# Kernel optimization log

Measured on AMD Instinct MI355X. Metric: run time of the kernel, lower is better.

## Reference

```python
import jax, jax.numpy as jnp
import numpy as np

B, C, H, W = 32, 256, 32, 32   # batch, channels (inplanes==planes), spatial
E = 8                          # num_experts
EPS = 1e-5                     # BatchNorm eps


def setup_inputs() -> dict:
    key = jax.random.key(0)
    ks = jax.random.split(key, 6)
    s = 0.05
    return {
        "x": jax.random.normal(ks[0], (B, C, H, W), dtype=jnp.float32),
        # router: GAP -> Linear(C, E) -> sigmoid
        "router_w": jax.random.normal(ks[1], (E, C), dtype=jnp.float32) * s,
        "router_b": jnp.zeros((E,), dtype=jnp.float32),
        # expert kernel banks for the two CondConv2d layers (OIHW per expert)
        "w1": jax.random.normal(ks[2], (E, C, C, 3, 3), dtype=jnp.float32) * s,
        "w2": jax.random.normal(ks[3], (E, C, C, 3, 3), dtype=jnp.float32) * s,
        # BatchNorm (eval mode: running stats) params for bn1/bn2
        "g1": jnp.ones((C,), jnp.float32), "b1": jnp.zeros((C,), jnp.float32),
        "m1": jnp.zeros((C,), jnp.float32), "v1": jnp.ones((C,), jnp.float32),
        "g2": jnp.ones((C,), jnp.float32), "b2": jnp.zeros((C,), jnp.float32),
        "m2": jnp.zeros((C,), jnp.float32), "v2": jnp.ones((C,), jnp.float32),
    }


def _bn(x, g, b, m, v):
    # eval-mode BatchNorm over channel dim 1
    scale = (g * jax.lax.rsqrt(v + EPS))[None, :, None, None]
    shift = (b - m * g * jax.lax.rsqrt(v + EPS))[None, :, None, None]
    return x * scale + shift


def _cond_conv(x, w_bank, r):
    # x: [B,C,H,W]; w_bank: [E,O,I,3,3]; r: [B,E]
    # combine expert kernels per sample, then per-sample 3x3 conv (pad=1, stride=1)
    k = jnp.einsum('be,eoihw->boihw', r, w_bank)  # [B,O,I,3,3]

    def one(xb, kb):
        return jax.lax.conv_general_dilated(
            xb[None], kb, window_strides=(1, 1), padding=[(1, 1), (1, 1)],
            dimension_numbers=('NCHW', 'OIHW', 'NCHW'))[0]

    return jax.vmap(one)(x, k)  # [B,O,H,W]


def reference(x, router_w, router_b, w1, w2, g1, b1, m1, v1, g2, b2, m2, v2):
    # BasicRouter: global average pool -> linear -> sigmoid
    r = jax.nn.sigmoid(jnp.mean(x, axis=(2, 3)) @ router_w.T + router_b)  # [B,E]
    # drop_expert is identity in eval mode (training=False)
    out = jax.nn.relu(_bn(_cond_conv(x, w1, r), g1, b1, m1, v1))
    out = _bn(_cond_conv(out, w2, r), g2, b2, m2, v2)
    return jax.nn.relu(out + x)  # identity residual (stride=1, inplanes==planes)
```

## Files before the change

kernel.cpp:

```cpp
#include <hip/hip_runtime.h>

typedef unsigned short ushort_t;
typedef __attribute__((ext_vector_type(8))) __bf16 bf16x8;
typedef __attribute__((ext_vector_type(4))) float f32x4;
typedef __attribute__((ext_vector_type(4))) int i32x4;
typedef __attribute__((ext_vector_type(4))) unsigned short u16x4;

#define BN_EPS 1e-5f
#define EPAD 136

#define BAR()    __builtin_amdgcn_s_barrier()
#define VMCNT4() asm volatile("s_waitcnt vmcnt(4)" ::: "memory")
#define VMCNT0() asm volatile("s_waitcnt vmcnt(0)" ::: "memory")
#define LGKM0()  asm volatile("s_waitcnt lgkmcnt(0)" ::: "memory")

__device__ __forceinline__ ushort_t f2bf(float f) {
    union { float f; unsigned u; } v; v.f = f;
    unsigned r = v.u + 0x7FFFu + ((v.u >> 16) & 1u);
    return (ushort_t)(r >> 16);
}
__device__ __forceinline__ float bf2f(ushort_t h) {
    union { unsigned u; float f; } v; v.u = ((unsigned)h) << 16; return v.f;
}

__device__ __forceinline__ void async_cp16(const ushort_t* g, ushort_t* l) {
    __builtin_amdgcn_global_load_lds(
        (const __attribute__((address_space(1))) unsigned int*)g,
        (__attribute__((address_space(3))) unsigned int*)l, 16, 0, 0);
}

__global__ void transpose_gap_kernel(const float* __restrict__ x, ushort_t* __restrict__ xt,
                                     float* __restrict__ gpart) {
    __shared__ float tile[32][33];
    int b = blockIdx.z, c0 = blockIdx.y * 32, p0 = blockIdx.x * 32;
    int t = threadIdx.x;
    int c = t >> 3, q = t & 7;
    f32x4 v = *(const f32x4*)(x + ((long)b * 256 + c0 + c) * 1024 + p0 + q * 4);
    tile[c][q * 4 + 0] = v[0];
    tile[c][q * 4 + 1] = v[1];
    tile[c][q * 4 + 2] = v[2];
    tile[c][q * 4 + 3] = v[3];
    float ps = v[0] + v[1] + v[2] + v[3];
    ps += __shfl_down(ps, 4, 8);
    ps += __shfl_down(ps, 2, 8);
    ps += __shfl_down(ps, 1, 8);
    if (q == 0) gpart[((long)b * 256 + c0 + c) * 32 + blockIdx.x] = ps;
    __syncthreads();
    int p = t >> 3, coff = (t & 7) * 4;
    u16x4 pk;
    #pragma unroll
    for (int i = 0; i < 4; ++i) pk[i] = f2bf(tile[coff + i][p]);
    *(u16x4*)(xt + ((long)b * 1024 + p0 + p) * 256 + c0 + coff) = pk;
}

__global__ void router_linear_kernel(const float* __restrict__ gpart, const float* __restrict__ rw,
                                     const float* __restrict__ rb, float* __restrict__ r) {
    int be = blockIdx.x;
    int b = be >> 3, e = be & 7;
    int lane = threadIdx.x;
    float s = 0.f;
    #pragma unroll
    for (int i = 0; i < 4; ++i) {
        int c = lane + i * 64;
        const f32x4* gp = (const f32x4*)(gpart + ((long)b * 256 + c) * 32);
        float g = 0.f;
        #pragma unroll
        for (int j = 0; j < 8; ++j) { f32x4 v = gp[j]; g += (v[0] + v[1]) + (v[2] + v[3]); }
        s += g * rw[e * 256 + c];
    }
    #pragma unroll
    for (int off = 32; off; off >>= 1) s += __shfl_down(s, off, 64);
    if (lane == 0) r[be] = 1.f / (1.f + expf(-(s * (1.f / 1024.f) + rb[e])));
}

__global__ __launch_bounds__(256, 2) void combine_kernel(const float* __restrict__ w,
                                                         const float* __restrict__ r,
                                                         ushort_t* __restrict__ ko) {
    __shared__ float wl[9216];
    ushort_t* outb = (ushort_t*)wl;
    const int t = threadIdx.x;
    const int g0 = blockIdx.x * 128;

    #pragma unroll
    for (int it = 0; it < 9; ++it) {
        int lin = it * 256 + t;
        int e = lin / 288, rem = lin - e * 288;
        f32x4 v = *(const f32x4*)(w + (long)e * 589824 + (long)g0 * 9 + rem * 4);
        *(f32x4*)(&wl[lin * 4]) = v;
    }
    __syncthreads();

    const int g = t & 127;
    const int half = t >> 7;
    float wv[8][9];
    #pragma unroll
    for (int e = 0; e < 8; ++e)
        #pragma unroll
        for (int p = 0; p < 9; ++p)
            wv[e][p] = wl[e * 1152 + g * 9 + p];
    __syncthreads();

    #pragma unroll
    for (int hb = 0; hb < 2; ++hb) {
        #pragma unroll
        for (int j = 0; j < 8; ++j) {
            int b16 = half * 8 + j;
            int b = hb * 16 + b16;
            float rv[8];
            #pragma unroll
            for (int e = 0; e < 8; ++e) rv[e] = r[b * 8 + e];
            #pragma unroll
            for (int p = 0; p < 9; ++p) {
                float s = 0.f;
                #pragma unroll
                for (int e = 0; e < 8; ++e) s += rv[e] * wv[e][p];
                outb[(b16 * 9 + p) * 128 + g] = f2bf(s);
            }
        }
        __syncthreads();
        #pragma unroll
        for (int it = 0; it < 9; ++it) {
            int idx = it * 256 + t;
            int row = idx >> 4, off = idx & 15;
            int b16 = row / 9, p = row - b16 * 9;
            i32x4 v = *(i32x4*)(&outb[row * 128 + off * 8]);
            *(i32x4*)(ko + ((long)((hb * 16 + b16) * 9 + p)) * 65536 + g0 + off * 8) = v;
        }
        __syncthreads();
    }
}

template <int MODE>
__global__ __launch_bounds__(256, 2) void gemm_conv(
    const ushort_t* __restrict__ xin,
    const ushort_t* __restrict__ kbank,
    void* __restrict__ outp,
    const float* __restrict__ gam, const float* __restrict__ bet,
    const float* __restrict__ mu, const float* __restrict__ var,
    const ushort_t* __restrict__ residt) {
    __shared__ ushort_t smem[37632];
    ushort_t* ldsB = smem;
    ushort_t* ldsA = smem + 13056;

    const int t = threadIdx.x;
    const int lane = t & 63;
    const int lane15 = lane & 15;
    const int quad = lane >> 4;
    const int wv = t >> 6;
    const int id = blockIdx.x;
    const int q  = id >> 3;
    const int mt = q & 1;
    const int nt = (q >> 1) & 7;
    const int b  = (id & 7) + ((q >> 4) << 3);
    const int h0 = nt * 4;
    const int p0 = nt * 128;
    const int mw0 = (wv >> 1) * 64;
    const int nw0 = (wv & 1) * 64;
    const int wbase = t & ~63;

    f32x4 acc[4][4];
    #pragma unroll
    for (int i = 0; i < 4; ++i)
        #pragma unroll
        for (int j = 0; j < 4; ++j) acc[i][j] = 0.f;

    if (t < 96) {
        int rix = t >> 3, j = t & 7;
        int pi = (rix >> 1) * 34 + (rix & 1) * 33;
        i32x4 z = 0;
        *(i32x4*)(&ldsB[(pi * 8 + j) * 8]) = z;
    }
    if (nt == 0) { i32x4 z = 0; *(i32x4*)(&ldsB[(8 + t) * 8]) = z; }
    if (nt == 7) { i32x4 z = 0; *(i32x4*)(&ldsB[((5 * 34 + 1) * 8 + t) * 8]) = z; }

    const long xbase = (long)b * 1024 * 256;
    const long kbase = (long)b * 9 * 65536;

    auto stageB = [&](int kc) {
        #pragma unroll
        for (int hh = 0; hh < 6; ++hh) {
            int hg = h0 + hh - 1;
            if (hg < 0 || hg >= 32) continue;
            int ww = t >> 3;
            int pi = hh * 34 + 1 + ww;
            int jd = (t & 7) ^ (pi & 7);
            async_cp16(xin + xbase + (long)(hg * 32 + ww) * 256 + kc * 64 + jd * 8,
                       ldsB + ((hh * 34 + 1) * 8 + wbase) * 8);
        }
    };
    auto stageA = [&](int kc, int pos, int buf) {
        const ushort_t* srcA = kbank + kbase + (long)pos * 65536 + (long)mt * 32768 + kc * 64;
        ushort_t* base = ldsA + buf * 8192;
        #pragma unroll
        for (int it = 0; it < 4; ++it) {
            int s = it * 256 + t;
            int row = s >> 3;
            int k8 = (s & 7) ^ (row & 7);
            async_cp16(srcA + (long)row * 256 + k8 * 8, base + (it * 256 + wbase) * 8);
        }
    };

    stageB(0);
    stageA(0, 0, 0);
    __syncthreads();

    int cur = 0;
    for (int kc = 0; kc < 4; ++kc) {
        for (int pos = 0; pos < 9; ++pos) {
            const bool last = (kc == 3 && pos == 8);
            const int nxt = (cur == 2) ? 0 : cur + 1;
            if (!last) {
                int nk = kc, np = pos + 1;
                if (np == 9) { np = 0; ++nk; }
                stageA(nk, np, nxt);
                VMCNT4();
            } else {
                VMCNT0();
            }
            BAR();

            const int dh = pos / 3 - 1, dw = pos % 3 - 1;
            const ushort_t* ab = ldsA + cur * 8192;
            bf16x8 af[2][4], bfr[2][4];
            #pragma unroll
            for (int kb = 0; kb < 2; ++kb) {
                int jk = kb * 4 + quad;
                #pragma unroll
                for (int mf = 0; mf < 4; ++mf) {
                    int row = mw0 + mf * 16 + lane15;
                    af[kb][mf] = *(const bf16x8*)(ab + (row * 8 + (jk ^ (row & 7))) * 8);
                }
                #pragma unroll
                for (int nf = 0; nf < 4; ++nf) {
                    int n = nw0 + nf * 16 + lane15;
                    int pi = ((n >> 5) + 1 + dh) * 34 + (n & 31) + 1 + dw;
                    bfr[kb][nf] = *(const bf16x8*)(&ldsB[(pi * 8 + (jk ^ (pi & 7))) * 8]);
                }
            }
            if (pos == 8 && kc < 3) {
                LGKM0();
                BAR();
                stageB(kc + 1);
            }

            __builtin_amdgcn_s_setprio(1);
            #pragma unroll
            for (int kb = 0; kb < 2; ++kb)
                #pragma unroll
                for (int mf = 0; mf < 4; ++mf)
                    #pragma unroll
                    for (int nf = 0; nf < 4; ++nf)
                        acc[mf][nf] = __builtin_amdgcn_mfma_f32_16x16x32_bf16(af[kb][mf], bfr[kb][nf], acc[mf][nf], 0, 0, 0);
            __builtin_amdgcn_s_setprio(0);
            LGKM0();
            cur = nxt;
        }
    }

    u16x4 rres[4][4];
    if (MODE == 1) {
        #pragma unroll
        for (int mf = 0; mf < 4; ++mf)
            #pragma unroll
            for (int nf = 0; nf < 4; ++nf) {
                int p = p0 + nw0 + nf * 16 + lane15;
                int cb = mt * 128 + mw0 + mf * 16 + quad * 4;
                rres[mf][nf] = *(const u16x4*)(residt + ((long)b * 1024 + p) * 256 + cb);
            }
    }

    float sc[4][4], sh[4][4];
    #pragma unroll
    for (int mf = 0; mf < 4; ++mf)
        #pragma unroll
        for (int i = 0; i < 4; ++i) {
            int c = mt * 128 + mw0 + mf * 16 + quad * 4 + i;
            float s = gam[c] * rsqrtf(var[c] + BN_EPS);
            sc[mf][i] = s;
            sh[mf][i] = bet[c] - mu[c] * s;
        }

    if (MODE == 0) {
        __syncthreads();
        ushort_t* ldsE = smem;
        #pragma unroll
        for (int mf = 0; mf < 4; ++mf)
            #pragma unroll
            for (int nf = 0; nf < 4; ++nf) {
                int pl = nw0 + nf * 16 + lane15;
                int cb = mw0 + mf * 16 + quad * 4;
                u16x4 pk;
                #pragma unroll
                for (int i = 0; i < 4; ++i) {
                    float v = acc[mf][nf][i] * sc[mf][i] + sh[mf][i];
                    pk[i] = f2bf(fmaxf(v, 0.f));
                }
                *(u16x4*)(&ldsE[pl * EPAD + cb]) = pk;
            }
        __syncthreads();
        ushort_t* op = (ushort_t*)outp;
        #pragma unroll
        for (int it = 0; it < 8; ++it) {
            int s = t + it * 256;
            int row = s >> 4, l16 = s & 15;
            i32x4 v = *(i32x4*)(&ldsE[row * EPAD + l16 * 8]);
            *(i32x4*)(op + ((long)b * 1024 + p0 + row) * 256 + mt * 128 + l16 * 8) = v;
        }
    } else {
        float* op = (float*)outp;
        #pragma unroll
        for (int mf = 0; mf < 4; ++mf)
            #pragma unroll
            for (int nf = 0; nf < 4; ++nf) {
                int p = p0 + nw0 + nf * 16 + lane15;
                #pragma unroll
                for (int i = 0; i < 4; ++i) {
                    int c = mt * 128 + mw0 + mf * 16 + quad * 4 + i;
                    float v = acc[mf][nf][i] * sc[mf][i] + sh[mf][i] + bf2f(rres[mf][nf][i]);
                    op[((long)b * 256 + c) * 1024 + p] = fmaxf(v, 0.f);
                }
            }
    }
}

extern "C" void kernel_launch(void* const* d_in, const int* in_sizes, int n_in,
                              void* d_out, int out_size, void* d_ws, size_t ws_size,
                              hipStream_t stream) {
    const float* x  = (const float*)d_in[0];
    const float* rw = (const float*)d_in[1];
    const float* rb = (const float*)d_in[2];
    const float* w1 = (const float*)d_in[3];
    const float* w2 = (const float*)d_in[4];
    const float* g1 = (const float*)d_in[5];
    const float* b1 = (const float*)d_in[6];
    const float* m1 = (const float*)d_in[7];
    const float* v1 = (const float*)d_in[8];
    const float* g2 = (const float*)d_in[9];
    const float* b2 = (const float*)d_in[10];
    const float* m2 = (const float*)d_in[11];
    const float* v2 = (const float*)d_in[12];

    const size_t GP_OFF  = 4096;
    const size_t XT_OFF  = GP_OFF + (size_t)1048576;
    const size_t O1_OFF  = XT_OFF + (size_t)16777216;
    const size_t KB_OFF  = O1_OFF + (size_t)16777216;
    const size_t NEED    = KB_OFF + (size_t)32 * 9 * 65536 * 2;
    if (ws_size < NEED) return;

    char* ws = (char*)d_ws;
    float* r       = (float*)ws;
    float* gpart   = (float*)(ws + GP_OFF);
    ushort_t* xt   = (ushort_t*)(ws + XT_OFF);
    ushort_t* o1   = (ushort_t*)(ws + O1_OFF);
    ushort_t* kbuf = (ushort_t*)(ws + KB_OFF);

    transpose_gap_kernel<<<dim3(32, 8, 32), 256, 0, stream>>>(x, xt, gpart);
    router_linear_kernel<<<256, 64, 0, stream>>>(gpart, rw, rb, r);
    combine_kernel<<<dim3(512), 256, 0, stream>>>(w1, r, kbuf);
    gemm_conv<0><<<512, 256, 0, stream>>>(xt, kbuf, (void*)o1, g1, b1, m1, v1, nullptr);
    combine_kernel<<<dim3(512), 256, 0, stream>>>(w2, r, kbuf);
    gemm_conv<1><<<512, 256, 0, stream>>>(o1, kbuf, d_out, g2, b2, m2, v2, xt);
}
```

Baseline: 227.4 us.

## Use two-wave blocks with 128x64 warp tiles and double-buffered weight staging

Shrinks the conv GEMM block from four waves to two, so each wave computes a 128x64 tile (8x4 MFMA fragments) instead of 64x64, and each A fragment is reused across more B columns. The weight pipeline goes from a triple buffer to a double buffer to cut LDS use, with an extra barrier every step to guard buffer reuse. This aims to raise MFMA work per LDS read, but doubles accumulator registers per thread and halves the waves per block. That can reduce latency hiding and may cause spills under the new launch bounds.

```diff
diff --git a/kernel.cpp b/kernel.cpp
--- a/kernel.cpp
+++ b/kernel.cpp
@@ -10,7 +10,7 @@
 #define EPAD 136
 
 #define BAR()    __builtin_amdgcn_s_barrier()
-#define VMCNT4() asm volatile("s_waitcnt vmcnt(4)" ::: "memory")
+#define VMCNT8() asm volatile("s_waitcnt vmcnt(8)" ::: "memory")
 #define VMCNT0() asm volatile("s_waitcnt vmcnt(0)" ::: "memory")
 #define LGKM0()  asm volatile("s_waitcnt lgkmcnt(0)" ::: "memory")
 
@@ -131,14 +131,14 @@
 }
 
 template <int MODE>
-__global__ __launch_bounds__(256, 2) void gemm_conv(
+__global__ __launch_bounds__(128, 1) void gemm_conv(
     const ushort_t* __restrict__ xin,
     const ushort_t* __restrict__ kbank,
     void* __restrict__ outp,
     const float* __restrict__ gam, const float* __restrict__ bet,
     const float* __restrict__ mu, const float* __restrict__ var,
     const ushort_t* __restrict__ residt) {
-    __shared__ ushort_t smem[37632];
+    __shared__ ushort_t smem[29440];
     ushort_t* ldsB = smem;
     ushort_t* ldsA = smem + 13056;
 
@@ -146,7 +146,7 @@
     const int lane = t & 63;
     const int lane15 = lane & 15;
     const int quad = lane >> 4;
-    const int wv = t >> 6;
+    const int wvi = t >> 6;
     const int id = blockIdx.x;
     const int q  = id >> 3;
     const int mt = q & 1;
@@ -154,13 +154,12 @@
     const int b  = (id & 7) + ((q >> 4) << 3);
     const int h0 = nt * 4;
     const int p0 = nt * 128;
-    const int mw0 = (wv >> 1) * 64;
-    const int nw0 = (wv & 1) * 64;
+    const int nw0 = wvi * 64;
     const int wbase = t & ~63;
 
-    f32x4 acc[4][4];
-    #pragma unroll
-    for (int i = 0; i < 4; ++i)
+    f32x4 acc[8][4];
+    #pragma unroll
+    for (int i = 0; i < 8; ++i)
         #pragma unroll
         for (int j = 0; j < 4; ++j) acc[i][j] = 0.f;
 
@@ -170,8 +169,16 @@
         i32x4 z = 0;
         *(i32x4*)(&ldsB[(pi * 8 + j) * 8]) = z;
     }
-    if (nt == 0) { i32x4 z = 0; *(i32x4*)(&ldsB[(8 + t) * 8]) = z; }
-    if (nt == 7) { i32x4 z = 0; *(i32x4*)(&ldsB[((5 * 34 + 1) * 8 + t) * 8]) = z; }
+    if (nt == 0) {
+        i32x4 z = 0;
+        *(i32x4*)(&ldsB[(8 + t) * 8]) = z;
+        *(i32x4*)(&ldsB[(8 + 128 + t) * 8]) = z;
+    }
+    if (nt == 7) {
+        i32x4 z = 0;
+        *(i32x4*)(&ldsB[((5 * 34 + 1) * 8 + t) * 8]) = z;
+        *(i32x4*)(&ldsB[((5 * 34 + 1) * 8 + 128 + t) * 8]) = z;
+    }
 
     const long xbase = (long)b * 1024 * 256;
     const long kbase = (long)b * 9 * 65536;
@@ -181,22 +188,26 @@
         for (int hh = 0; hh < 6; ++hh) {
             int hg = h0 + hh - 1;
             if (hg < 0 || hg >= 32) continue;
-            int ww = t >> 3;
-            int pi = hh * 34 + 1 + ww;
-            int jd = (t & 7) ^ (pi & 7);
-            async_cp16(xin + xbase + (long)(hg * 32 + ww) * 256 + kc * 64 + jd * 8,
-                       ldsB + ((hh * 34 + 1) * 8 + wbase) * 8);
+            #pragma unroll
+            for (int rr = 0; rr < 2; ++rr) {
+                int s = rr * 128 + t;
+                int ww = s >> 3;
+                int pi = hh * 34 + 1 + ww;
+                int jd = (s & 7) ^ (pi & 7);
+                async_cp16(xin + xbase + (long)(hg * 32 + ww) * 256 + kc * 64 + jd * 8,
+                           ldsB + ((hh * 34 + 1) * 8 + rr * 128 + wbase) * 8);
+            }
         }
     };
     auto stageA = [&](int kc, int pos, int buf) {
         const ushort_t* srcA = kbank + kbase + (long)pos * 65536 + (long)mt * 32768 + kc * 64;
         ushort_t* base = ldsA + buf * 8192;
         #pragma unroll
-        for (int it = 0; it < 4; ++it) {
-            int s = it * 256 + t;
+        for (int it = 0; it < 8; ++it) {
+            int s = it * 128 + t;
             int row = s >> 3;
             int k8 = (s & 7) ^ (row & 7);
-            async_cp16(srcA + (long)row * 256 + k8 * 8, base + (it * 256 + wbase) * 8);
+            async_cp16(srcA + (long)row * 256 + k8 * 8, base + (it * 128 + wbase) * 8);
         }
     };
 
@@ -204,30 +215,31 @@
     stageA(0, 0, 0);
     __syncthreads();
 
-    int cur = 0;
+    int par = 0;
+    #pragma unroll 1
     for (int kc = 0; kc < 4; ++kc) {
+        #pragma unroll 1
         for (int pos = 0; pos < 9; ++pos) {
             const bool last = (kc == 3 && pos == 8);
-            const int nxt = (cur == 2) ? 0 : cur + 1;
             if (!last) {
                 int nk = kc, np = pos + 1;
                 if (np == 9) { np = 0; ++nk; }
-                stageA(nk, np, nxt);
-                VMCNT4();
+                stageA(nk, np, par ^ 1);
+                VMCNT8();
             } else {
                 VMCNT0();
             }
             BAR();
 
             const int dh = pos / 3 - 1, dw = pos % 3 - 1;
-            const ushort_t* ab = ldsA + cur * 8192;
-            bf16x8 af[2][4], bfr[2][4];
+            const ushort_t* ab = ldsA + par * 8192;
+            bf16x8 af[2][8], bfr[2][4];
             #pragma unroll
             for (int kb = 0; kb < 2; ++kb) {
                 int jk = kb * 4 + quad;
                 #pragma unroll
-                for (int mf = 0; mf < 4; ++mf) {
-                    int row = mw0 + mf * 16 + lane15;
+                for (int mf = 0; mf < 8; ++mf) {
+                    int row = mf * 16 + lane15;
                     af[kb][mf] = *(const bf16x8*)(ab + (row * 8 + (jk ^ (row & 7))) * 8);
                 }
                 #pragma unroll
@@ -237,44 +249,42 @@
                     bfr[kb][nf] = *(const bf16x8*)(&ldsB[(pi * 8 + (jk ^ (pi & 7))) * 8]);
                 }
             }
-            if (pos == 8 && kc < 3) {
-                LGKM0();
-                BAR();
-                stageB(kc + 1);
-            }
+            LGKM0();
+            BAR();
+
+            if (pos == 8 && kc < 3) stageB(kc + 1);
 
             __builtin_amdgcn_s_setprio(1);
             #pragma unroll
             for (int kb = 0; kb < 2; ++kb)
                 #pragma unroll
-                for (int mf = 0; mf < 4; ++mf)
+                for (int mf = 0; mf < 8; ++mf)
                     #pragma unroll
                     for (int nf = 0; nf < 4; ++nf)
                         acc[mf][nf] = __builtin_amdgcn_mfma_f32_16x16x32_bf16(af[kb][mf], bfr[kb][nf], acc[mf][nf], 0, 0, 0);
             __builtin_amdgcn_s_setprio(0);
-            LGKM0();
-            cur = nxt;
-        }
-    }
-
-    u16x4 rres[4][4];
+            par ^= 1;
+        }
+    }
+
+    u16x4 rres[8][4];
     if (MODE == 1) {
         #pragma unroll
-        for (int mf = 0; mf < 4; ++mf)
+        for (int mf = 0; mf < 8; ++mf)
             #pragma unroll
             for (int nf = 0; nf < 4; ++nf) {
                 int p = p0 + nw0 + nf * 16 + lane15;
-                int cb = mt * 128 + mw0 + mf * 16 + quad * 4;
+                int cb = mt * 128 + mf * 16 + quad * 4;
                 rres[mf][nf] = *(const u16x4*)(residt + ((long)b * 1024 + p) * 256 + cb);
             }
     }
 
-    float sc[4][4], sh[4][4];
-    #pragma unroll
-    for (int mf = 0; mf < 4; ++mf)
+    float sc[8][4], sh[8][4];
+    #pragma unroll
+    for (int mf = 0; mf < 8; ++mf)
         #pragma unroll
         for (int i = 0; i < 4; ++i) {
-            int c = mt * 128 + mw0 + mf * 16 + quad * 4 + i;
+            int c = mt * 128 + mf * 16 + quad * 4 + i;
             float s = gam[c] * rsqrtf(var[c] + BN_EPS);
             sc[mf][i] = s;
             sh[mf][i] = bet[c] - mu[c] * s;
@@ -284,11 +294,11 @@
         __syncthreads();
         ushort_t* ldsE = smem;
         #pragma unroll
-        for (int mf = 0; mf < 4; ++mf)
+        for (int mf = 0; mf < 8; ++mf)
             #pragma unroll
             for (int nf = 0; nf < 4; ++nf) {
                 int pl = nw0 + nf * 16 + lane15;
-                int cb = mw0 + mf * 16 + quad * 4;
+                int cb = mf * 16 + quad * 4;
                 u16x4 pk;
                 #pragma unroll
                 for (int i = 0; i < 4; ++i) {
@@ -300,8 +310,8 @@
         __syncthreads();
         ushort_t* op = (ushort_t*)outp;
         #pragma unroll
-        for (int it = 0; it < 8; ++it) {
-            int s = t + it * 256;
+        for (int it = 0; it < 16; ++it) {
+            int s = t + it * 128;
             int row = s >> 4, l16 = s & 15;
             i32x4 v = *(i32x4*)(&ldsE[row * EPAD + l16 * 8]);
             *(i32x4*)(op + ((long)b * 1024 + p0 + row) * 256 + mt * 128 + l16 * 8) = v;
@@ -309,13 +319,13 @@
     } else {
         float* op = (float*)outp;
         #pragma unroll
-        for (int mf = 0; mf < 4; ++mf)
+        for (int mf = 0; mf < 8; ++mf)
             #pragma unroll
             for (int nf = 0; nf < 4; ++nf) {
                 int p = p0 + nw0 + nf * 16 + lane15;
                 #pragma unroll
                 for (int i = 0; i < 4; ++i) {
-                    int c = mt * 128 + mw0 + mf * 16 + quad * 4 + i;
+                    int c = mt * 128 + mf * 16 + quad * 4 + i;
                     float v = acc[mf][nf][i] * sc[mf][i] + sh[mf][i] + bf2f(rres[mf][nf][i]);
                     op[((long)b * 256 + c) * 1024 + p] = fmaxf(v, 0.f);
                 }
@@ -357,7 +367,7 @@
     transpose_gap_kernel<<<dim3(32, 8, 32), 256, 0, stream>>>(x, xt, gpart);
     router_linear_kernel<<<256, 64, 0, stream>>>(gpart, rw, rb, r);
     combine_kernel<<<dim3(512), 256, 0, stream>>>(w1, r, kbuf);
-    gemm_conv<0><<<512, 256, 0, stream>>>(xt, kbuf, (void*)o1, g1, b1, m1, v1, nullptr);
+    gemm_conv<0><<<512, 128, 0, stream>>>(xt, kbuf, (void*)o1, g1, b1, m1, v1, nullptr);
     combine_kernel<<<dim3(512), 256, 0, stream>>>(w2, r, kbuf);
-    gemm_conv<1><<<512, 256, 0, stream>>>(o1, kbuf, d_out, g2, b2, m2, v2, xt);
-}
+    gemm_conv<1><<<512, 128, 0, stream>>>(o1, kbuf, d_out, g2, b2, m2, v2, xt);
+}
```

New measurement: 248.8 us. +9.4%, slower.
